# Kernel optimization log

Hardware: AMD Instinct MI355X
Metric: run time of the kernel (lower is better)

The kernel has to match this reference:

```python
import jax, jax.numpy as jnp
import numpy as np

N_NODES = 50000
N_EDGES = 800000
IN_CH = 128
HID = 64
HEADS = 4
OUT_CH = 1
NEG_SLOPE = 0.2  # PyG GATConv default


def setup_inputs() -> dict:
    key = jax.random.key(0)
    ks = jax.random.split(key, 16)
    s = 0.1
    x = jax.random.normal(ks[0], (N_NODES, IN_CH), dtype=jnp.float32)
    edge_index = jax.random.randint(ks[1], (2, N_EDGES), 0, N_NODES, dtype=jnp.int64)
    # GATConv 1: in=128 -> 64 per head, 4 heads, concat
    W1 = jax.random.normal(ks[2], (IN_CH, HEADS * HID), dtype=jnp.float32) * s
    att_src1 = jax.random.normal(ks[3], (HEADS, HID), dtype=jnp.float32) * s
    att_dst1 = jax.random.normal(ks[4], (HEADS, HID), dtype=jnp.float32) * s
    b1 = jnp.zeros((HEADS * HID,), dtype=jnp.float32)
    # GATConv 2: in=256 -> 64, 1 head, mean (concat=False)
    W2 = jax.random.normal(ks[5], (HEADS * HID, HID), dtype=jnp.float32) * s
    att_src2 = jax.random.normal(ks[6], (1, HID), dtype=jnp.float32) * s
    att_dst2 = jax.random.normal(ks[7], (1, HID), dtype=jnp.float32) * s
    b2 = jnp.zeros((HID,), dtype=jnp.float32)
    # MLP: Linear(128,64) -> ReLU -> Linear(64,1)
    mlp_w1 = jax.random.normal(ks[8], (2 * HID, HID), dtype=jnp.float32) * s
    mlp_b1 = jnp.zeros((HID,), dtype=jnp.float32)
    mlp_w2 = jax.random.normal(ks[9], (HID, OUT_CH), dtype=jnp.float32) * s
    mlp_b2 = jnp.zeros((OUT_CH,), dtype=jnp.float32)
    return dict(x=x, edge_index=edge_index, W1=W1, att_src1=att_src1,
                att_dst1=att_dst1, b1=b1, W2=W2, att_src2=att_src2,
                att_dst2=att_dst2, b2=b2, mlp_w1=mlp_w1, mlp_b1=mlp_b1,
                mlp_w2=mlp_w2, mlp_b2=mlp_b2)


def gat_layer(x, edge_index, W, att_src, att_dst, bias, heads, ch, concat):
    N = x.shape[0]
    # add self loops (PyG default add_self_loops=True)
    loop = jnp.arange(N, dtype=edge_index.dtype)
    src = jnp.concatenate([edge_index[0], loop])
    dst = jnp.concatenate([edge_index[1], loop])
    h = (x @ W).reshape(N, heads, ch)                      # [N,H,C]
    a_src = jnp.einsum('nhc,hc->nh', h, att_src)           # [N,H]
    a_dst = jnp.einsum('nhc,hc->nh', h, att_dst)
    logits = jax.nn.leaky_relu(a_src[src] + a_dst[dst], NEG_SLOPE)  # [E,H]
    # segment softmax over destination node
    m = jax.ops.segment_max(logits, dst, num_segments=N)
    e = jnp.exp(logits - m[dst])
    denom = jax.ops.segment_sum(e, dst, num_segments=N)
    alpha = e / denom[dst]                                 # [E,H]
    msg = alpha[:, :, None] * h[src]                       # [E,H,C]
    out = jax.ops.segment_sum(msg, dst, num_segments=N)    # [N,H,C]
    out = out.reshape(N, heads * ch) if concat else out.mean(axis=1)
    return out + bias


def reference(x, edge_index, W1, att_src1, att_dst1, b1,
              W2, att_src2, att_dst2, b2,
              mlp_w1, mlp_b1, mlp_w2, mlp_b2):
    # eval mode: dropouts are identity
    h = gat_layer(x, edge_index, W1, att_src1, att_dst1, b1, HEADS, HID, True)
    h = jax.nn.elu(h)
    h = gat_layer(h, edge_index, W2, att_src2, att_dst2, b2, 1, HID, False)
    u = h[edge_index[0]]                                   # [E,HID]
    v = h[edge_index[1]]
    ef = jnp.concatenate([u, v], axis=1)                   # [E,2*HID]
    hid = jax.nn.relu(ef @ mlp_w1 + mlp_b1)
    return hid @ mlp_w2 + mlp_b2                           # [E,OUT_CH]
```

## Files before the change

### kernel.cpp

```cpp
#include <hip/hip_runtime.h>
#include <hip/hip_bf16.h>
#include <math.h>

#define NN 50000
#define NE 800000
#define NB ((NN + 255) / 256)
#define NEG 0.2f
#define NHB ((NE + 255) / 256)

typedef __hip_bfloat16 bf16;
typedef __attribute__((ext_vector_type(8))) short s8v;
typedef __attribute__((ext_vector_type(4))) float f4v;

__device__ __forceinline__ float bf2f(unsigned short u) {
  union { unsigned int i; float f; } c;
  c.i = ((unsigned int)u) << 16;
  return c.f;
}
__device__ __forceinline__ float blo(unsigned int u) {
  union { unsigned int i; float f; } c;
  c.i = u << 16;
  return c.f;
}
__device__ __forceinline__ float bhi(unsigned int u) {
  union { unsigned int i; float f; } c;
  c.i = u & 0xffff0000u;
  return c.f;
}
__device__ __forceinline__ unsigned short f2b(float f) {
  bf16 b = __float2bfloat16(f);
  return __builtin_bit_cast(unsigned short, b);
}
__device__ __forceinline__ float lrelu(float t) { return (t > 0.f) ? t : NEG * t; }

#define NX4 (NN * 32)
#define NW1 (256 * 128)
#define NW2 (64 * 256)
#define NPQ (128 * 64)
__global__ void prep_k(const int* __restrict__ ei, int* __restrict__ counts,
                       const float* __restrict__ x, const float* __restrict__ W1,
                       const float* __restrict__ W2, const float* __restrict__ mw1,
                       unsigned short* __restrict__ xb, unsigned short* __restrict__ w1t,
                       unsigned short* __restrict__ w2t, unsigned short* __restrict__ pqt) {
  int b = blockIdx.x;
  if (b < NHB) {
    int e = b * 256 + threadIdx.x;
    if (e < NE) atomicAdd(&counts[ei[NE + e]], 1);
    return;
  }
  int i = (b - NHB) * 256 + threadIdx.x;
  if (i < NX4) {
    float4 v = *(const float4*)(x + (size_t)i * 4);
    ushort4 o = {f2b(v.x), f2b(v.y), f2b(v.z), f2b(v.w)};
    *(ushort4*)(xb + (size_t)i * 4) = o;
    return;
  }
  i -= NX4;
  if (i < NW1) {
    int n = i >> 7, k = i & 127;
    w1t[i] = f2b(W1[(size_t)k * 256 + n]);
    return;
  }
  i -= NW1;
  if (i < NW2) {
    int n = i >> 8, k = i & 255;
    w2t[i] = f2b(W2[(size_t)k * 64 + n]);
    return;
  }
  i -= NW2;
  if (i < NPQ) {
    int n = i >> 6, k = i & 63;
    float v = (n < 64) ? mw1[(size_t)k * 64 + n] : mw1[(size_t)(64 + k) * 64 + (n - 64)];
    pqt[i] = f2b(v);
  }
}

__global__ __launch_bounds__(256) void scan_bsum_k(const int* __restrict__ counts,
                                                   int* __restrict__ bsums) {
  __shared__ int wsum[4];
  int i = blockIdx.x * 256 + threadIdx.x;
  int v = (i < NN) ? counts[i] : 0;
#pragma unroll
  for (int off = 32; off; off >>= 1) v += __shfl_xor(v, off);
  if ((threadIdx.x & 63) == 0) wsum[threadIdx.x >> 6] = v;
  __syncthreads();
  if (threadIdx.x == 0) bsums[blockIdx.x] = wsum[0] + wsum[1] + wsum[2] + wsum[3];
}

__global__ __launch_bounds__(256) void scan_final_k(const int* __restrict__ counts,
                                                    const int* __restrict__ bsums,
                                                    int* __restrict__ offsets,
                                                    int* __restrict__ cur_lo,
                                                    int* __restrict__ cur_hi) {
  __shared__ int s[256];
  __shared__ int wsum[4];
  __shared__ int bpref;
  int t = threadIdx.x;
  int bv = (t < NB && t < (int)blockIdx.x) ? bsums[t] : 0;
#pragma unroll
  for (int off = 32; off; off >>= 1) bv += __shfl_xor(bv, off);
  if ((t & 63) == 0) wsum[t >> 6] = bv;
  __syncthreads();
  if (t == 0) bpref = wsum[0] + wsum[1] + wsum[2] + wsum[3];
  int i = blockIdx.x * 256 + t;
  int v = (i < NN) ? counts[i] : 0;
  s[t] = v;
  __syncthreads();
  for (int off = 1; off < 256; off <<= 1) {
    int u = (t >= off) ? s[t - off] : 0;
    __syncthreads();
    s[t] += u;
    __syncthreads();
  }
  int excl = s[t] - v + bpref;
  if (i < NN) {
    offsets[i] = excl;
    cur_lo[i] = excl;
    cur_hi[i] = excl + v - 1;
    if (i == NN - 1) offsets[NN] = excl + v;
  }
}

__global__ void scatter_k(const int* __restrict__ ei, int* __restrict__ cur_lo,
                          int* __restrict__ cur_hi, int2* __restrict__ csr) {
  int e = blockIdx.x * 256 + threadIdx.x;
  if (e >= NE) return;
  int s = ei[e], d = ei[NE + e];
  int pos = (s < NN / 2) ? atomicAdd(&cur_lo[d], 1) : atomicSub(&cur_hi[d], 1);
  csr[pos] = make_int2(s, e);
}

template <int DOTS>
__global__ __launch_bounds__(256) void mgemm_k(
    const unsigned short* __restrict__ A, int lda,
    const unsigned short* __restrict__ Bt, int ldb,
    unsigned short* __restrict__ C, int ldc,
    int M, int N, int K,
    const float* __restrict__ ws, const float* __restrict__ wd,
    float* __restrict__ as_, float* __restrict__ ad_, int H) {
  __shared__ unsigned short Asl[64][40];
  __shared__ unsigned short Btl[64][40];
  __shared__ float sdot[64], ddot[64];
  int bm = blockIdx.y * 64, bn = blockIdx.x * 64;
  int t = threadIdx.x;
  int wv = t >> 6, lane = t & 63;
  int wm = (wv >> 1) * 32, wn = (wv & 1) * 32;
  int l16 = lane & 15, lq = lane >> 4;
  if (DOTS && t < 64) { sdot[t] = 0.f; ddot[t] = 0.f; }
  f4v acc[2][2];
#pragma unroll
  for (int mi = 0; mi < 2; ++mi)
#pragma unroll
    for (int ni = 0; ni < 2; ++ni) {
      acc[mi][ni][0] = 0.f; acc[mi][ni][1] = 0.f;
      acc[mi][ni][2] = 0.f; acc[mi][ni][3] = 0.f;
    }
  int sr = t >> 2, sc = (t & 3) * 8;
  for (int k0 = 0; k0 < K; k0 += 32) {
    uint4 av = {0, 0, 0, 0};
    int gr = bm + sr;
    if (gr < M) av = *(const uint4*)(A + (size_t)gr * lda + k0 + sc);
    *(uint4*)&Asl[sr][sc] = av;
    uint4 bv = *(const uint4*)(Bt + (size_t)(bn + sr) * ldb + k0 + sc);
    *(uint4*)&Btl[sr][sc] = bv;
    __syncthreads();
    s8v af[2], bfv[2];
#pragma unroll
    for (int mi = 0; mi < 2; ++mi)
      af[mi] = *(const s8v*)&Asl[wm + mi * 16 + l16][lq * 8];
#pragma unroll
    for (int ni = 0; ni < 2; ++ni)
      bfv[ni] = *(const s8v*)&Btl[wn + ni * 16 + l16][lq * 8];
#pragma unroll
    for (int mi = 0; mi < 2; ++mi)
#pragma unroll
      for (int ni = 0; ni < 2; ++ni)
        acc[mi][ni] = __builtin_amdgcn_mfma_f32_16x16x32_bf16(
            af[mi], bfv[ni], acc[mi][ni], 0, 0, 0);
    __syncthreads();
  }
#pragma unroll
  for (int mi = 0; mi < 2; ++mi)
#pragma unroll
    for (int rr = 0; rr < 4; ++rr) {
      int row = bm + wm + mi * 16 + lq * 4 + rr;
      if (row < M) {
#pragma unroll
        for (int ni = 0; ni < 2; ++ni) {
          int col = bn + wn + ni * 16 + l16;
          C[(size_t)row * ldc + col] = f2b(acc[mi][ni][rr]);
        }
      }
    }
  if (DOTS) {
    int head = blockIdx.x;
    float ps[2][4], pd[2][4];
#pragma unroll
    for (int mi = 0; mi < 2; ++mi)
#pragma unroll
      for (int rr = 0; rr < 4; ++rr) {
        float s = 0.f, d = 0.f;
#pragma unroll
        for (int ni = 0; ni < 2; ++ni) {
          int col = wn + ni * 16 + l16;
          s += acc[mi][ni][rr] * ws[head * 64 + col];
          d += acc[mi][ni][rr] * wd[head * 64 + col];
        }
        ps[mi][rr] = s;
        pd[mi][rr] = d;
      }
#pragma unroll
    for (int off = 1; off < 16; off <<= 1)
#pragma unroll
      for (int mi = 0; mi < 2; ++mi)
#pragma unroll
        for (int rr = 0; rr < 4; ++rr) {
          ps[mi][rr] += __shfl_xor(ps[mi][rr], off);
          pd[mi][rr] += __shfl_xor(pd[mi][rr], off);
        }
    if (l16 == 0) {
#pragma unroll
      for (int mi = 0; mi < 2; ++mi)
#pragma unroll
        for (int rr = 0; rr < 4; ++rr) {
          int rl = wm + mi * 16 + lq * 4 + rr;
          atomicAdd(&sdot[rl], ps[mi][rr]);
          atomicAdd(&ddot[rl], pd[mi][rr]);
        }
    }
    __syncthreads();
    if (t < 64 && bm + t < M) {
      as_[(size_t)(bm + t) * H + head] = sdot[t];
      ad_[(size_t)(bm + t) * H + head] = ddot[t];
    }
  }
}

__global__ __launch_bounds__(256) void gat_agg4_k(
    const int* __restrict__ offsets, const int2* __restrict__ csr,
    const unsigned short* __restrict__ h, const float* __restrict__ as_,
    const float* __restrict__ ad_, const float* __restrict__ bias,
    unsigned short* __restrict__ out) {
  __shared__ float exs[4][64][4];
  __shared__ int srcs[4][64];
  int wvx = threadIdx.x >> 6, lane = threadIdx.x & 63;
  int n = blockIdx.x * 4 + wvx;
  int hd = lane >> 4;
  int beg = offsets[n], end = offsets[n + 1];
  float4 adn = *(const float4*)(ad_ + (size_t)n * 4);
  float4 asn = *(const float4*)(as_ + (size_t)n * 4);
  float es0 = __expf(lrelu(asn.x + adn.x));
  float es1 = __expf(lrelu(asn.y + adn.y));
  float es2 = __expf(lrelu(asn.z + adn.z));
  float es3 = __expf(lrelu(asn.w + adn.w));
  float d0 = es0, d1 = es1, d2 = es2, d3 = es3;
  float wself = (hd == 0) ? es0 : (hd == 1) ? es1 : (hd == 2) ? es2 : es3;
  uint2 sv = *(const uint2*)(h + (size_t)n * 256 + lane * 4);
  float2 a01, a23;
  a01.x = wself * blo(sv.x); a01.y = wself * bhi(sv.x);
  a23.x = wself * blo(sv.y); a23.y = wself * bhi(sv.y);
  for (int base = beg; base < end; base += 64) {
    int cnt = min(64, end - base);
    int src = 0;
    float e0 = 0.f, e1 = 0.f, e2 = 0.f, e3 = 0.f;
    if (lane < cnt) {
      src = csr[base + lane].x;
      float4 a4 = *(const float4*)(as_ + (size_t)src * 4);
      e0 = __expf(lrelu(a4.x + adn.x));
      e1 = __expf(lrelu(a4.y + adn.y));
      e2 = __expf(lrelu(a4.z + adn.z));
      e3 = __expf(lrelu(a4.w + adn.w));
    }
    float s0 = e0, s1 = e1, s2 = e2, s3 = e3;
#pragma unroll
    for (int off = 32; off; off >>= 1) {
      s0 += __shfl_xor(s0, off);
      s1 += __shfl_xor(s1, off);
      s2 += __shfl_xor(s2, off);
      s3 += __shfl_xor(s3, off);
    }
    d0 += s0; d1 += s1; d2 += s2; d3 += s3;
    float4 ex4 = {e0, e1, e2, e3};
    *(float4*)(&exs[wvx][lane][0]) = ex4;
    srcs[wvx][lane] = src;
    __builtin_amdgcn_wave_barrier();
    int e = 0;
    for (; e + 8 <= cnt; e += 8) {
      uint2 r[8];
      float w[8];
#pragma unroll
      for (int j = 0; j < 8; ++j) {
        int si = srcs[wvx][e + j];
        w[j] = exs[wvx][e + j][hd];
        r[j] = *(const uint2*)(h + (size_t)si * 256 + lane * 4);
      }
#pragma unroll
      for (int j = 0; j < 8; ++j) {
        a01.x += w[j] * blo(r[j].x); a01.y += w[j] * bhi(r[j].x);
        a23.x += w[j] * blo(r[j].y); a23.y += w[j] * bhi(r[j].y);
      }
    }
    for (; e < cnt; ++e) {
      int si = srcs[wvx][e];
      float w = exs[wvx][e][hd];
      uint2 r = *(const uint2*)(h + (size_t)si * 256 + lane * 4);
      a01.x += w * blo(r.x); a01.y += w * bhi(r.x);
      a23.x += w * blo(r.y); a23.y += w * bhi(r.y);
    }
  }
  float myden = (hd == 0) ? d0 : (hd == 1) ? d1 : (hd == 2) ? d2 : d3;
  float inv = 1.f / myden;
  float4 b4 = *(const float4*)(bias + lane * 4);
  float4 res;
  res.x = a01.x * inv + b4.x;
  res.y = a01.y * inv + b4.y;
  res.z = a23.x * inv + b4.z;
  res.w = a23.y * inv + b4.w;
  res.x = (res.x > 0.f) ? res.x : (__expf(res.x) - 1.f);
  res.y = (res.y > 0.f) ? res.y : (__expf(res.y) - 1.f);
  res.z = (res.z > 0.f) ? res.z : (__expf(res.z) - 1.f);
  res.w = (res.w > 0.f) ? res.w : (__expf(res.w) - 1.f);
  ushort4 ov = {f2b(res.x), f2b(res.y), f2b(res.z), f2b(res.w)};
  *(ushort4*)(out + (size_t)n * 256 + lane * 4) = ov;
}

__global__ __launch_bounds__(256) void gat_agg1_k(
    const int* __restrict__ offsets, const int2* __restrict__ csr,
    const unsigned short* __restrict__ h, const float* __restrict__ as_,
    const float* __restrict__ ad_, const float* __restrict__ bias,
    unsigned short* __restrict__ out) {
  __shared__ float exs[4][64];
  __shared__ int srcs[4][64];
  int wvx = threadIdx.x >> 6, lane = threadIdx.x & 63;
  int n = blockIdx.x * 4 + wvx;
  int slot = lane >> 4, cp = lane & 15;
  int beg = offsets[n], end = offsets[n + 1];
  float adn = ad_[n];
  float eself = __expf(lrelu(as_[n] + adn));
  float den = eself;
  float2 a01 = {0.f, 0.f}, a23 = {0.f, 0.f};
  if (slot == 0) {
    uint2 sv = *(const uint2*)(h + (size_t)n * 64 + cp * 4);
    a01.x = eself * blo(sv.x); a01.y = eself * bhi(sv.x);
    a23.x = eself * blo(sv.y); a23.y = eself * bhi(sv.y);
  }
  for (int base = beg; base < end; base += 64) {
    int cnt = min(64, end - base);
    int src = 0;
    float ex = 0.f;
    if (lane < cnt) {
      src = csr[base + lane].x;
      ex = __expf(lrelu(as_[src] + adn));
    }
    float s = ex;
#pragma unroll
    for (int off = 32; off; off >>= 1) s += __shfl_xor(s, off);
    den += s;
    exs[wvx][lane] = ex;
    srcs[wvx][lane] = src;
    __builtin_amdgcn_wave_barrier();
    int i = slot;
    for (; i + 12 < cnt; i += 16) {
      uint2 r[4];
      int i0 = i, i1 = i + 4, i2 = i + 8, i3 = i + 12;
      r[0] = *(const uint2*)(h + (size_t)srcs[wvx][i0] * 64 + cp * 4);
      r[1] = *(const uint2*)(h + (size_t)srcs[wvx][i1] * 64 + cp * 4);
      r[2] = *(const uint2*)(h + (size_t)srcs[wvx][i2] * 64 + cp * 4);
      r[3] = *(const uint2*)(h + (size_t)srcs[wvx][i3] * 64 + cp * 4);
      float w0 = exs[wvx][i0], w1 = exs[wvx][i1], w2 = exs[wvx][i2], w3 = exs[wvx][i3];
      a01.x += w0 * blo(r[0].x); a01.y += w0 * bhi(r[0].x);
      a23.x += w0 * blo(r[0].y); a23.y += w0 * bhi(r[0].y);
      a01.x += w1 * blo(r[1].x); a01.y += w1 * bhi(r[1].x);
      a23.x += w1 * blo(r[1].y); a23.y += w1 * bhi(r[1].y);
      a01.x += w2 * blo(r[2].x); a01.y += w2 * bhi(r[2].x);
      a23.x += w2 * blo(r[2].y); a23.y += w2 * bhi(r[2].y);
      a01.x += w3 * blo(r[3].x); a01.y += w3 * bhi(r[3].x);
      a23.x += w3 * blo(r[3].y); a23.y += w3 * bhi(r[3].y);
    }
    for (; i < cnt; i += 4) {
      int si = srcs[wvx][i];
      float w = exs[wvx][i];
      uint2 r = *(const uint2*)(h + (size_t)si * 64 + cp * 4);
      a01.x += w * blo(r.x); a01.y += w * bhi(r.x);
      a23.x += w * blo(r.y); a23.y += w * bhi(r.y);
    }
  }
#pragma unroll
  for (int off = 16; off <= 32; off <<= 1) {
    a01.x += __shfl_xor(a01.x, off);
    a01.y += __shfl_xor(a01.y, off);
    a23.x += __shfl_xor(a23.x, off);
    a23.y += __shfl_xor(a23.y, off);
  }
  if (slot == 0) {
    float inv = 1.f / den;
    float4 b4 = *(const float4*)(bias + cp * 4);
    ushort4 ov;
    ov.x = f2b(a01.x * inv + b4.x);
    ov.y = f2b(a01.y * inv + b4.y);
    ov.z = f2b(a23.x * inv + b4.z);
    ov.w = f2b(a23.y * inv + b4.w);
    *(ushort4*)(out + (size_t)n * 64 + cp * 4) = ov;
  }
}

__global__ __launch_bounds__(256) void edge_out_k(
    const int* __restrict__ offsets, const int2* __restrict__ csr,
    const unsigned short* __restrict__ pq,
    const float* __restrict__ mb1, const float* __restrict__ w2,
    const float* __restrict__ mb2, float* __restrict__ out) {
  int wvx = threadIdx.x >> 6, lane = threadIdx.x & 63;
  int n = blockIdx.x * 4 + wvx;
  int slot = lane >> 4, cp = lane & 15;
  int beg = offsets[n], end = offsets[n + 1];
  ushort4 qv = *(const ushort4*)(pq + (size_t)n * 128 + 64 + cp * 4);
  float4 base4 = *(const float4*)(mb1 + cp * 4);
  base4.x += bf2f(qv.x); base4.y += bf2f(qv.y);
  base4.z += bf2f(qv.z); base4.w += bf2f(qv.w);
  float4 w4 = *(const float4*)(w2 + cp * 4);
  float b2v = mb2[0];
  for (int base = beg; base < end; base += 8) {
    int i0 = base + slot, i1 = base + 4 + slot;
    bool ok0 = (i0 < end), ok1 = (i1 < end);
    int2 se0 = {0, 0}, se1 = {0, 0};
    if (ok0) se0 = csr[i0];
    if (ok1) se1 = csr[i1];
    float r0 = 0.f, r1 = 0.f;
    if (ok0) {
      ushort4 pv = *(const ushort4*)(pq + (size_t)se0.x * 128 + cp * 4);
      float v0 = fmaxf(bf2f(pv.x) + base4.x, 0.f);
      float v1 = fmaxf(bf2f(pv.y) + base4.y, 0.f);
      float v2 = fmaxf(bf2f(pv.z) + base4.z, 0.f);
      float v3 = fmaxf(bf2f(pv.w) + base4.w, 0.f);
      r0 = v0 * w4.x + v1 * w4.y + v2 * w4.z + v3 * w4.w;
    }
    if (ok1) {
      ushort4 pv = *(const ushort4*)(pq + (size_t)se1.x * 128 + cp * 4);
      float v0 = fmaxf(bf2f(pv.x) + base4.x, 0.f);
      float v1 = fmaxf(bf2f(pv.y) + base4.y, 0.f);
      float v2 = fmaxf(bf2f(pv.z) + base4.z, 0.f);
      float v3 = fmaxf(bf2f(pv.w) + base4.w, 0.f);
      r1 = v0 * w4.x + v1 * w4.y + v2 * w4.z + v3 * w4.w;
    }
#pragma unroll
    for (int off = 8; off; off >>= 1) {
      r0 += __shfl_xor(r0, off);
      r1 += __shfl_xor(r1, off);
    }
    if (cp == 0) {
      if (ok0) out[se0.y] = r0 + b2v;
      if (ok1) out[se1.y] = r1 + b2v;
    }
  }
}

extern "C" void kernel_launch(void* const* d_in, const int* in_sizes, int n_in,
                              void* d_out, int out_size, void* d_ws, size_t ws_size,
                              hipStream_t stream) {
  const float* x = (const float*)d_in[0];
  const int* ei = (const int*)d_in[1];
  const float* W1 = (const float*)d_in[2];
  const float* as1w = (const float*)d_in[3];
  const float* ad1w = (const float*)d_in[4];
  const float* b1 = (const float*)d_in[5];
  const float* W2 = (const float*)d_in[6];
  const float* as2w = (const float*)d_in[7];
  const float* ad2w = (const float*)d_in[8];
  const float* b2 = (const float*)d_in[9];
  const float* mw1 = (const float*)d_in[10];
  const float* mb1 = (const float*)d_in[11];
  const float* mw2 = (const float*)d_in[12];
  const float* mb2 = (const float*)d_in[13];
  float* out = (float*)d_out;

  char* ws = (char*)d_ws;
  size_t o = 0;
  auto alloc = [&](size_t bytes) {
    void* ptr = ws + o;
    o += (bytes + 255) & ~(size_t)255;
    return ptr;
  };
  int* counts = (int*)alloc((size_t)NN * 4);
  int* offsets = (int*)alloc((size_t)(NN + 1) * 4);
  int* cur_lo = (int*)alloc((size_t)NN * 4);
  int* cur_hi = (int*)alloc((size_t)NN * 4);
  int* bsums = (int*)alloc((size_t)NB * 4);
  int2* csr = (int2*)alloc((size_t)NE * 8);
  unsigned short* xb = (unsigned short*)alloc((size_t)NN * 128 * 2);
  unsigned short* w1t = (unsigned short*)alloc((size_t)256 * 128 * 2);
  unsigned short* w2t = (unsigned short*)alloc((size_t)64 * 256 * 2);
  unsigned short* pqt = (unsigned short*)alloc((size_t)128 * 64 * 2);
  unsigned short* h1b = (unsigned short*)alloc((size_t)NN * 256 * 2);
  float* a_s1 = (float*)alloc((size_t)NN * 4 * 4);
  float* a_d1 = (float*)alloc((size_t)NN * 4 * 4);
  unsigned short* x2b = (unsigned short*)alloc((size_t)NN * 256 * 2);
  unsigned short* yb = (unsigned short*)alloc((size_t)NN * 64 * 2);
  unsigned short* h2b = h1b;
  unsigned short* pq = h1b + (size_t)NN * 64;

  hipMemsetAsync(counts, 0, (size_t)NN * 4, stream);
  prep_k<<<NHB + (NX4 + NW1 + NW2 + NPQ + 255) / 256, 256, 0, stream>>>(
      ei, counts, x, W1, W2, mw1, xb, w1t, w2t, pqt);
  scan_bsum_k<<<NB, 256, 0, stream>>>(counts, bsums);
  scan_final_k<<<NB, 256, 0, stream>>>(counts, bsums, offsets, cur_lo, cur_hi);
  scatter_k<<<(NE + 255) / 256, 256, 0, stream>>>(ei, cur_lo, cur_hi, csr);

  int gy = (NN + 63) / 64;
  mgemm_k<1><<<dim3(4, gy), 256, 0, stream>>>(xb, 128, w1t, 128, h1b, 256,
                                              NN, 256, 128, as1w, ad1w, a_s1, a_d1, 4);
  gat_agg4_k<<<NN / 4, 256, 0, stream>>>(offsets, csr, h1b, a_s1, a_d1, b1, x2b);

  mgemm_k<1><<<dim3(1, gy), 256, 0, stream>>>(x2b, 256, w2t, 256, h2b, 64,
                                              NN, 64, 256, as2w, ad2w, a_s1, a_d1, 1);
  gat_agg1_k<<<NN / 4, 256, 0, stream>>>(offsets, csr, h2b, a_s1, a_d1, b2, yb);

  mgemm_k<0><<<dim3(2, gy), 256, 0, stream>>>(yb, 64, pqt, 64, pq, 128,
                                              NN, 128, 64, nullptr, nullptr,
                                              nullptr, nullptr, 0);

  edge_out_k<<<NN / 4, 256, 0, stream>>>(offsets, csr, pq, mb1, mw2, mb2, out);
}
```

Before: 286.8 us.

## Aggregate raw inputs before layer-1 projection to shrink gather width

Layer one now computes attention logits directly from x using precomputed W1·att vectors. It aggregates the 128-wide bf16 input features per head (alpha-weighted sum of x[src]) and only then multiplies by W1 per head, fusing bias and ELU into that GEMM. The edge gather reads 128-channel rows instead of 256-channel projected rows, which roughly halves gather traffic. In exchange it writes a 512-wide per-head intermediate and adds extra kernels. The CSR scatter is also simplified to a single cursor, which drops the lo/hi split ordering by source.

```diff
diff --git a/kernel.cpp b/kernel.cpp
--- a/kernel.cpp
+++ b/kernel.cpp
@@ -75,6 +75,43 @@
   }
 }
 
+__global__ void attw_k(const float* __restrict__ W1, const float* __restrict__ as1w,
+                       const float* __restrict__ ad1w, float* __restrict__ watt) {
+  int b = blockIdx.x;
+  int h = b & 3, sel = b >> 2;
+  const float* att = (sel ? ad1w : as1w) + h * 64;
+  int k = threadIdx.x;
+  float s = 0.f;
+#pragma unroll 8
+  for (int c = 0; c < 64; ++c) s += W1[(size_t)k * 256 + h * 64 + c] * att[c];
+  watt[(sel * 4 + h) * 128 + k] = s;
+}
+
+__global__ __launch_bounds__(256) void attdot1_k(
+    const float* __restrict__ x, const float* __restrict__ watt,
+    float* __restrict__ as_, float* __restrict__ ad_) {
+  __shared__ float wsl[8][128];
+  int t = threadIdx.x;
+  for (int i = t; i < 1024; i += 256) ((float*)wsl)[i] = watt[i];
+  __syncthreads();
+  int wv = t >> 6, lane = t & 63;
+  int n = blockIdx.x * 4 + wv;
+  float2 xv = *(const float2*)(x + (size_t)n * 128 + lane * 2);
+  float r[8];
+#pragma unroll
+  for (int j = 0; j < 8; ++j)
+    r[j] = xv.x * wsl[j][lane * 2] + xv.y * wsl[j][lane * 2 + 1];
+#pragma unroll
+  for (int off = 32; off; off >>= 1) {
+#pragma unroll
+    for (int j = 0; j < 8; ++j) r[j] += __shfl_xor(r[j], off);
+  }
+  if (lane == 0) {
+    *(float4*)(as_ + (size_t)n * 4) = make_float4(r[0], r[1], r[2], r[3]);
+    *(float4*)(ad_ + (size_t)n * 4) = make_float4(r[4], r[5], r[6], r[7]);
+  }
+}
+
 __global__ __launch_bounds__(256) void scan_bsum_k(const int* __restrict__ counts,
                                                    int* __restrict__ bsums) {
   __shared__ int wsum[4];
@@ -90,8 +127,7 @@
 __global__ __launch_bounds__(256) void scan_final_k(const int* __restrict__ counts,
                                                     const int* __restrict__ bsums,
                                                     int* __restrict__ offsets,
-                                                    int* __restrict__ cur_lo,
-                                                    int* __restrict__ cur_hi) {
+                                                    int* __restrict__ cursor) {
   __shared__ int s[256];
   __shared__ int wsum[4];
   __shared__ int bpref;
@@ -115,18 +151,17 @@
   int excl = s[t] - v + bpref;
   if (i < NN) {
     offsets[i] = excl;
-    cur_lo[i] = excl;
-    cur_hi[i] = excl + v - 1;
+    cursor[i] = excl;
     if (i == NN - 1) offsets[NN] = excl + v;
   }
 }
 
-__global__ void scatter_k(const int* __restrict__ ei, int* __restrict__ cur_lo,
-                          int* __restrict__ cur_hi, int2* __restrict__ csr) {
+__global__ void scatter_k(const int* __restrict__ ei, int* __restrict__ cursor,
+                          int2* __restrict__ csr) {
   int e = blockIdx.x * 256 + threadIdx.x;
   if (e >= NE) return;
   int s = ei[e], d = ei[NE + e];
-  int pos = (s < NN / 2) ? atomicAdd(&cur_lo[d], 1) : atomicSub(&cur_hi[d], 1);
+  int pos = atomicAdd(&cursor[d], 1);
   csr[pos] = make_int2(s, e);
 }
 
@@ -236,16 +271,77 @@
   }
 }
 
-__global__ __launch_bounds__(256) void gat_agg4_k(
+__global__ __launch_bounds__(256) void mgemm_hx2_k(
+    const unsigned short* __restrict__ A,
+    const unsigned short* __restrict__ w1t,
+    const float* __restrict__ bias,
+    unsigned short* __restrict__ C) {
+  __shared__ unsigned short Asl[64][40];
+  __shared__ unsigned short Btl[64][40];
+  int head = blockIdx.x;
+  int bm = blockIdx.y * 64;
+  int t = threadIdx.x;
+  int wv = t >> 6, lane = t & 63;
+  int wm = (wv >> 1) * 32, wn = (wv & 1) * 32;
+  int l16 = lane & 15, lq = lane >> 4;
+  f4v acc[2][2];
+#pragma unroll
+  for (int mi = 0; mi < 2; ++mi)
+#pragma unroll
+    for (int ni = 0; ni < 2; ++ni) {
+      acc[mi][ni][0] = 0.f; acc[mi][ni][1] = 0.f;
+      acc[mi][ni][2] = 0.f; acc[mi][ni][3] = 0.f;
+    }
+  int sr = t >> 2, sc = (t & 3) * 8;
+  for (int k0 = 0; k0 < 128; k0 += 32) {
+    uint4 av = {0, 0, 0, 0};
+    int gr = bm + sr;
+    if (gr < NN) av = *(const uint4*)(A + (size_t)gr * 512 + head * 128 + k0 + sc);
+    *(uint4*)&Asl[sr][sc] = av;
+    uint4 bv = *(const uint4*)(w1t + (size_t)(head * 64 + sr) * 128 + k0 + sc);
+    *(uint4*)&Btl[sr][sc] = bv;
+    __syncthreads();
+    s8v af[2], bfv[2];
+#pragma unroll
+    for (int mi = 0; mi < 2; ++mi)
+      af[mi] = *(const s8v*)&Asl[wm + mi * 16 + l16][lq * 8];
+#pragma unroll
+    for (int ni = 0; ni < 2; ++ni)
+      bfv[ni] = *(const s8v*)&Btl[wn + ni * 16 + l16][lq * 8];
+#pragma unroll
+    for (int mi = 0; mi < 2; ++mi)
+#pragma unroll
+      for (int ni = 0; ni < 2; ++ni)
+        acc[mi][ni] = __builtin_amdgcn_mfma_f32_16x16x32_bf16(
+            af[mi], bfv[ni], acc[mi][ni], 0, 0, 0);
+    __syncthreads();
+  }
+#pragma unroll
+  for (int mi = 0; mi < 2; ++mi)
+#pragma unroll
+    for (int rr = 0; rr < 4; ++rr) {
+      int row = bm + wm + mi * 16 + lq * 4 + rr;
+      if (row < NN) {
+#pragma unroll
+        for (int ni = 0; ni < 2; ++ni) {
+          int col = head * 64 + wn + ni * 16 + l16;
+          float v = acc[mi][ni][rr] + bias[col];
+          v = (v > 0.f) ? v : (__expf(v) - 1.f);
+          C[(size_t)row * 256 + col] = f2b(v);
+        }
+      }
+    }
+}
+
+__global__ __launch_bounds__(256) void gat_aggx_k(
     const int* __restrict__ offsets, const int2* __restrict__ csr,
-    const unsigned short* __restrict__ h, const float* __restrict__ as_,
-    const float* __restrict__ ad_, const float* __restrict__ bias,
-    unsigned short* __restrict__ out) {
+    const unsigned short* __restrict__ xb, const float* __restrict__ as_,
+    const float* __restrict__ ad_, unsigned short* __restrict__ aggx) {
   __shared__ float exs[4][64][4];
   __shared__ int srcs[4][64];
   int wvx = threadIdx.x >> 6, lane = threadIdx.x & 63;
   int n = blockIdx.x * 4 + wvx;
-  int hd = lane >> 4;
+  int slot = lane >> 5, cp = lane & 31;
   int beg = offsets[n], end = offsets[n + 1];
   float4 adn = *(const float4*)(ad_ + (size_t)n * 4);
   float4 asn = *(const float4*)(as_ + (size_t)n * 4);
@@ -254,11 +350,19 @@
   float es2 = __expf(lrelu(asn.z + adn.z));
   float es3 = __expf(lrelu(asn.w + adn.w));
   float d0 = es0, d1 = es1, d2 = es2, d3 = es3;
-  float wself = (hd == 0) ? es0 : (hd == 1) ? es1 : (hd == 2) ? es2 : es3;
-  uint2 sv = *(const uint2*)(h + (size_t)n * 256 + lane * 4);
-  float2 a01, a23;
-  a01.x = wself * blo(sv.x); a01.y = wself * bhi(sv.x);
-  a23.x = wself * blo(sv.y); a23.y = wself * bhi(sv.y);
+  float acc[4][4];
+#pragma unroll
+  for (int h = 0; h < 4; ++h)
+#pragma unroll
+    for (int c = 0; c < 4; ++c) acc[h][c] = 0.f;
+  if (slot == 0) {
+    uint2 sv = *(const uint2*)(xb + (size_t)n * 128 + cp * 4);
+    float x0 = blo(sv.x), x1 = bhi(sv.x), x2 = blo(sv.y), x3 = bhi(sv.y);
+    acc[0][0] = es0 * x0; acc[0][1] = es0 * x1; acc[0][2] = es0 * x2; acc[0][3] = es0 * x3;
+    acc[1][0] = es1 * x0; acc[1][1] = es1 * x1; acc[1][2] = es1 * x2; acc[1][3] = es1 * x3;
+    acc[2][0] = es2 * x0; acc[2][1] = es2 * x1; acc[2][2] = es2 * x2; acc[2][3] = es2 * x3;
+    acc[3][0] = es3 * x0; acc[3][1] = es3 * x1; acc[3][2] = es3 * x2; acc[3][3] = es3 * x3;
+  }
   for (int base = beg; base < end; base += 64) {
     int cnt = min(64, end - base);
     int src = 0;
@@ -284,44 +388,59 @@
     *(float4*)(&exs[wvx][lane][0]) = ex4;
     srcs[wvx][lane] = src;
     __builtin_amdgcn_wave_barrier();
-    int e = 0;
-    for (; e + 8 <= cnt; e += 8) {
-      uint2 r[8];
-      float w[8];
-#pragma unroll
-      for (int j = 0; j < 8; ++j) {
-        int si = srcs[wvx][e + j];
-        w[j] = exs[wvx][e + j][hd];
-        r[j] = *(const uint2*)(h + (size_t)si * 256 + lane * 4);
+    int i = slot;
+    for (; i + 6 < cnt; i += 8) {
+      uint2 r[4];
+      float4 w[4];
+#pragma unroll
+      for (int j = 0; j < 4; ++j) {
+        int e = i + 2 * j;
+        r[j] = *(const uint2*)(xb + (size_t)srcs[wvx][e] * 128 + cp * 4);
+        w[j] = *(const float4*)(&exs[wvx][e][0]);
       }
 #pragma unroll
-      for (int j = 0; j < 8; ++j) {
-        a01.x += w[j] * blo(r[j].x); a01.y += w[j] * bhi(r[j].x);
-        a23.x += w[j] * blo(r[j].y); a23.y += w[j] * bhi(r[j].y);
+      for (int j = 0; j < 4; ++j) {
+        float x0 = blo(r[j].x), x1 = bhi(r[j].x), x2 = blo(r[j].y), x3 = bhi(r[j].y);
+        acc[0][0] += w[j].x * x0; acc[0][1] += w[j].x * x1;
+        acc[0][2] += w[j].x * x2; acc[0][3] += w[j].x * x3;
+        acc[1][0] += w[j].y * x0; acc[1][1] += w[j].y * x1;
+        acc[1][2] += w[j].y * x2; acc[1][3] += w[j].y * x3;
+        acc[2][0] += w[j].z * x0; acc[2][1] += w[j].z * x1;
+        acc[2][2] += w[j].z * x2; acc[2][3] += w[j].z * x3;
+        acc[3][0] += w[j].w * x0; acc[3][1] += w[j].w * x1;
+        acc[3][2] += w[j].w * x2; acc[3][3] += w[j].w * x3;
       }
     }
-    for (; e < cnt; ++e) {
-      int si = srcs[wvx][e];
-      float w = exs[wvx][e][hd];
-      uint2 r = *(const uint2*)(h + (size_t)si * 256 + lane * 4);
-      a01.x += w * blo(r.x); a01.y += w * bhi(r.x);
-      a23.x += w * blo(r.y); a23.y += w * bhi(r.y);
-    }
-  }
-  float myden = (hd == 0) ? d0 : (hd == 1) ? d1 : (hd == 2) ? d2 : d3;
-  float inv = 1.f / myden;
-  float4 b4 = *(const float4*)(bias + lane * 4);
-  float4 res;
-  res.x = a01.x * inv + b4.x;
-  res.y = a01.y * inv + b4.y;
-  res.z = a23.x * inv + b4.z;
-  res.w = a23.y * inv + b4.w;
-  res.x = (res.x > 0.f) ? res.x : (__expf(res.x) - 1.f);
-  res.y = (res.y > 0.f) ? res.y : (__expf(res.y) - 1.f);
-  res.z = (res.z > 0.f) ? res.z : (__expf(res.z) - 1.f);
-  res.w = (res.w > 0.f) ? res.w : (__expf(res.w) - 1.f);
-  ushort4 ov = {f2b(res.x), f2b(res.y), f2b(res.z), f2b(res.w)};
-  *(ushort4*)(out + (size_t)n * 256 + lane * 4) = ov;
+    for (; i < cnt; i += 2) {
+      uint2 r = *(const uint2*)(xb + (size_t)srcs[wvx][i] * 128 + cp * 4);
+      float4 w = *(const float4*)(&exs[wvx][i][0]);
+      float x0 = blo(r.x), x1 = bhi(r.x), x2 = blo(r.y), x3 = bhi(r.y);
+      acc[0][0] += w.x * x0; acc[0][1] += w.x * x1; acc[0][2] += w.x * x2; acc[0][3] += w.x * x3;
+      acc[1][0] += w.y * x0; acc[1][1] += w.y * x1; acc[1][2] += w.y * x2; acc[1][3] += w.y * x3;
+      acc[2][0] += w.z * x0; acc[2][1] += w.z * x1; acc[2][2] += w.z * x2; acc[2][3] += w.z * x3;
+      acc[3][0] += w.w * x0; acc[3][1] += w.w * x1; acc[3][2] += w.w * x2; acc[3][3] += w.w * x3;
+    }
+  }
+#pragma unroll
+  for (int h = 0; h < 4; ++h)
+#pragma unroll
+    for (int c = 0; c < 4; ++c) acc[h][c] += __shfl_xor(acc[h][c], 32);
+  if (slot == 0) {
+    float inv0 = 1.f / d0, inv1 = 1.f / d1, inv2 = 1.f / d2, inv3 = 1.f / d3;
+    ushort4 o0 = {f2b(acc[0][0] * inv0), f2b(acc[0][1] * inv0),
+                  f2b(acc[0][2] * inv0), f2b(acc[0][3] * inv0)};
+    ushort4 o1 = {f2b(acc[1][0] * inv1), f2b(acc[1][1] * inv1),
+                  f2b(acc[1][2] * inv1), f2b(acc[1][3] * inv1)};
+    ushort4 o2 = {f2b(acc[2][0] * inv2), f2b(acc[2][1] * inv2),
+                  f2b(acc[2][2] * inv2), f2b(acc[2][3] * inv2)};
+    ushort4 o3 = {f2b(acc[3][0] * inv3), f2b(acc[3][1] * inv3),
+                  f2b(acc[3][2] * inv3), f2b(acc[3][3] * inv3)};
+    size_t rb = (size_t)n * 512 + cp * 4;
+    *(ushort4*)(aggx + rb) = o0;
+    *(ushort4*)(aggx + rb + 128) = o1;
+    *(ushort4*)(aggx + rb + 256) = o2;
+    *(ushort4*)(aggx + rb + 384) = o3;
+  }
 }
 
 __global__ __launch_bounds__(256) void gat_agg1_k(
@@ -482,33 +601,35 @@
   };
   int* counts = (int*)alloc((size_t)NN * 4);
   int* offsets = (int*)alloc((size_t)(NN + 1) * 4);
-  int* cur_lo = (int*)alloc((size_t)NN * 4);
-  int* cur_hi = (int*)alloc((size_t)NN * 4);
+  int* cursor = (int*)alloc((size_t)NN * 4);
   int* bsums = (int*)alloc((size_t)NB * 4);
   int2* csr = (int2*)alloc((size_t)NE * 8);
   unsigned short* xb = (unsigned short*)alloc((size_t)NN * 128 * 2);
   unsigned short* w1t = (unsigned short*)alloc((size_t)256 * 128 * 2);
   unsigned short* w2t = (unsigned short*)alloc((size_t)64 * 256 * 2);
   unsigned short* pqt = (unsigned short*)alloc((size_t)128 * 64 * 2);
-  unsigned short* h1b = (unsigned short*)alloc((size_t)NN * 256 * 2);
+  float* watt = (float*)alloc((size_t)8 * 128 * 4);
+  unsigned short* big = (unsigned short*)alloc((size_t)NN * 512 * 2);
   float* a_s1 = (float*)alloc((size_t)NN * 4 * 4);
   float* a_d1 = (float*)alloc((size_t)NN * 4 * 4);
   unsigned short* x2b = (unsigned short*)alloc((size_t)NN * 256 * 2);
   unsigned short* yb = (unsigned short*)alloc((size_t)NN * 64 * 2);
-  unsigned short* h2b = h1b;
-  unsigned short* pq = h1b + (size_t)NN * 64;
+  unsigned short* aggx = big;
+  unsigned short* h2b = big;
+  unsigned short* pq = big + (size_t)NN * 64;
 
   hipMemsetAsync(counts, 0, (size_t)NN * 4, stream);
   prep_k<<<NHB + (NX4 + NW1 + NW2 + NPQ + 255) / 256, 256, 0, stream>>>(
       ei, counts, x, W1, W2, mw1, xb, w1t, w2t, pqt);
+  attw_k<<<8, 128, 0, stream>>>(W1, as1w, ad1w, watt);
   scan_bsum_k<<<NB, 256, 0, stream>>>(counts, bsums);
-  scan_final_k<<<NB, 256, 0, stream>>>(counts, bsums, offsets, cur_lo, cur_hi);
-  scatter_k<<<(NE + 255) / 256, 256, 0, stream>>>(ei, cur_lo, cur_hi, csr);
+  scan_final_k<<<NB, 256, 0, stream>>>(counts, bsums, offsets, cursor);
+  scatter_k<<<(NE + 255) / 256, 256, 0, stream>>>(ei, cursor, csr);
 
   int gy = (NN + 63) / 64;
-  mgemm_k<1><<<dim3(4, gy), 256, 0, stream>>>(xb, 128, w1t, 128, h1b, 256,
-                                              NN, 256, 128, as1w, ad1w, a_s1, a_d1, 4);
-  gat_agg4_k<<<NN / 4, 256, 0, stream>>>(offsets, csr, h1b, a_s1, a_d1, b1, x2b);
+  attdot1_k<<<NN / 4, 256, 0, stream>>>(x, watt, a_s1, a_d1);
+  gat_aggx_k<<<NN / 4, 256, 0, stream>>>(offsets, csr, xb, a_s1, a_d1, aggx);
+  mgemm_hx2_k<<<dim3(4, gy), 256, 0, stream>>>(aggx, w1t, b1, x2b);
 
   mgemm_k<1><<<dim3(1, gy), 256, 0, stream>>>(x2b, 256, w2t, 256, h2b, 64,
                                               NN, 64, 256, as2w, ad2w, a_s1, a_d1, 1);
```

New measurement: 297.1 us. +3.6%, slower.
